# Optimization experiments

Hardware: AMD Instinct MI355X
Metric: run time of the kernel (lower is better)

## Reference

```python
import jax, jax.numpy as jnp
import numpy as np

HEADS = 48
HEAD_DIM = 64
DIM = 3072
RANK = 128
TEXT_LEN = 226
VID_LEN = 1822
B = 1
LORA_W = 1.0
EPS = 1e-5


def setup_inputs() -> dict:
    key = jax.random.key(0)
    ks = jax.random.split(key, 24)
    s = 0.02  # weight init scale
    inp = {
        "hidden_states": jax.random.normal(ks[0], (B, VID_LEN, DIM), jnp.float32),
        "encoder_hidden_states": jax.random.normal(ks[1], (B, TEXT_LEN, DIM), jnp.float32),
        "rope_cos": jax.random.uniform(ks[2], (VID_LEN, HEAD_DIM), jnp.float32),
        "rope_sin": jax.random.uniform(ks[3], (VID_LEN, HEAD_DIM), jnp.float32),
        "Wq": jax.random.normal(ks[4], (DIM, DIM), jnp.float32) * s,
        "bq": jax.random.normal(ks[5], (DIM,), jnp.float32) * s,
        "Wk": jax.random.normal(ks[6], (DIM, DIM), jnp.float32) * s,
        "bk": jax.random.normal(ks[7], (DIM,), jnp.float32) * s,
        "Wv": jax.random.normal(ks[8], (DIM, DIM), jnp.float32) * s,
        "bv": jax.random.normal(ks[9], (DIM,), jnp.float32) * s,
        "Wo": jax.random.normal(ks[10], (DIM, DIM), jnp.float32) * s,
        "bo": jax.random.normal(ks[11], (DIM,), jnp.float32) * s,
        "lq_down": jax.random.normal(ks[12], (RANK, DIM), jnp.float32) / RANK,
        "lq_up": jax.random.normal(ks[13], (DIM, RANK), jnp.float32) * s,
        "lk_down": jax.random.normal(ks[14], (RANK, DIM), jnp.float32) / RANK,
        "lk_up": jax.random.normal(ks[15], (DIM, RANK), jnp.float32) * s,
        "lv_down": jax.random.normal(ks[16], (RANK, DIM), jnp.float32) / RANK,
        "lv_up": jax.random.normal(ks[17], (DIM, RANK), jnp.float32) * s,
        "lp_down": jax.random.normal(ks[18], (RANK, DIM), jnp.float32) / RANK,
        "lp_up": jax.random.normal(ks[19], (DIM, RANK), jnp.float32) * s,
        "gamma_q": jnp.ones((HEAD_DIM,), jnp.float32),
        "beta_q": jnp.zeros((HEAD_DIM,), jnp.float32),
        "gamma_k": jnp.ones((HEAD_DIM,), jnp.float32),
        "beta_k": jnp.zeros((HEAD_DIM,), jnp.float32),
    }
    return inp


def _lora(x, down, up):
    # x: [B,S,DIM]; down: [RANK,DIM]; up: [DIM,RANK]
    return (x @ down.T) @ up.T


def _layernorm(x, gamma, beta):
    mu = jnp.mean(x, axis=-1, keepdims=True)
    var = jnp.mean(jnp.square(x - mu), axis=-1, keepdims=True)
    return (x - mu) * jax.lax.rsqrt(var + EPS) * gamma + beta


def _apply_rope(x, cos, sin):
    # diffusers apply_rotary_emb, use_real=True, unbind_dim=-1
    # x: [B,H,S,D]; cos/sin: [S,D]
    xr = x.reshape(*x.shape[:-1], HEAD_DIM // 2, 2)
    x1, x2 = xr[..., 0], xr[..., 1]
    x_rot = jnp.stack([-x2, x1], axis=-1).reshape(x.shape)
    return x * cos + x_rot * sin


def reference(hidden_states, encoder_hidden_states, rope_cos, rope_sin,
              Wq, bq, Wk, bk, Wv, bv, Wo, bo,
              lq_down, lq_up, lk_down, lk_up, lv_down, lv_up, lp_down, lp_up,
              gamma_q, beta_q, gamma_k, beta_k):
    h = jnp.concatenate([encoder_hidden_states, hidden_states], axis=1)  # [B,S,DIM]
    S = h.shape[1]

    q = h @ Wq.T + bq + _lora(h, lq_down, lq_up) * LORA_W
    k = h @ Wk.T + bk + _lora(h, lk_down, lk_up) * LORA_W
    v = h @ Wv.T + bv + _lora(h, lv_down, lv_up) * LORA_W

    def split_heads(x):  # [B,S,DIM] -> [B,H,S,D]
        return x.reshape(B, S, HEADS, HEAD_DIM).transpose(0, 2, 1, 3)

    q, k, v = split_heads(q), split_heads(k), split_heads(v)
    q = _layernorm(q, gamma_q, beta_q)
    k = _layernorm(k, gamma_k, beta_k)

    # RoPE on video tokens only
    q = q.at[:, :, TEXT_LEN:].set(_apply_rope(q[:, :, TEXT_LEN:], rope_cos, rope_sin))
    k = k.at[:, :, TEXT_LEN:].set(_apply_rope(k[:, :, TEXT_LEN:], rope_cos, rope_sin))

    # scaled dot-product attention (no mask, no dropout)
    scale = 1.0 / np.sqrt(HEAD_DIM).astype(np.float32)
    scores = jnp.einsum("bhqd,bhkd->bhqk", q, k) * scale
    probs = jax.nn.softmax(scores, axis=-1)
    attn_out = jnp.einsum("bhqk,bhkd->bhqd", probs, v)

    out = attn_out.transpose(0, 2, 1, 3).reshape(B, S, DIM)
    out = out @ Wo.T + bo + _lora(out, lp_down, lp_up) * LORA_W

    enc_out = out[:, :TEXT_LEN, :]
    hid_out = out[:, TEXT_LEN:, :]
    return (hid_out, enc_out)
```

## Files before the change

kernel.cpp:

```cpp
#include <hip/hip_runtime.h>
#include <hip/hip_bf16.h>
#include <stdint.h>

#define S_TOT 2048
#define TEXT 226
#define VID 1822
#define DIM 3072
#define NH 48
#define HD 64

typedef __bf16 bf16x8 __attribute__((ext_vector_type(8)));
typedef __bf16 bf16x4 __attribute__((ext_vector_type(4)));
typedef float f32x4 __attribute__((ext_vector_type(4)));

#define AS1 __attribute__((address_space(1)))
#define AS3 __attribute__((address_space(3)))

__device__ __forceinline__ void g2l16(const void* g, void* l) {
    __builtin_amdgcn_global_load_lds((const AS1 uint32_t*)(uintptr_t)g,
                                     (AS3 uint32_t*)(uintptr_t)l, 16, 0, 0);
}

__device__ __forceinline__ f32x4 mfma16(bf16x4 a, bf16x4 b, f32x4 c) {
#if __has_builtin(__builtin_amdgcn_mfma_f32_16x16x16bf16_1k)
    typedef short s4 __attribute__((ext_vector_type(4)));
    union U { bf16x4 b; s4 s; };
    U ua, ub; ua.b = a; ub.b = b;
    return __builtin_amdgcn_mfma_f32_16x16x16bf16_1k(ua.s, ub.s, c, 0, 0, 0);
#else
    f32x4 d = c;
    asm volatile("v_mfma_f32_16x16x16_bf16 %0, %1, %2, %0"
                 : "+v"(d) : "v"(a), "v"(b));
    return d;
#endif
}

#define ARENA_N 47431680ull

struct NormArgs { const void* p[24]; };

__global__ __launch_bounds__(256)
void normalize_inputs(NormArgs a, __bf16* __restrict__ arena)
{
    static constexpr unsigned long long segStart[25] = {
        0ull, 694272ull, 6291456ull, 15728640ull, 25165824ull, 34603008ull,
        44040192ull, 44433408ull, 44826624ull, 45219840ull, 45613056ull,
        46006272ull, 46399488ull, 46792704ull, 47185920ull, 47302528ull,
        47419136ull, 47422208ull, 47425280ull, 47428352ull, 47431424ull,
        47431488ull, 47431552ull, 47431616ull, 47431680ull };
    static constexpr int segIn[24] = {
        1, 0, 4, 6, 8, 10, 12, 13, 14, 15, 16, 17, 18, 19, 2, 3,
        5, 7, 9, 11, 20, 21, 22, 23 };

    const uint32_t w0 = *(const uint32_t*)a.p[20];
    const bool f32in = (w0 == 0x3F800000u);

    const size_t i0 = ((size_t)blockIdx.x * 256 + threadIdx.x) * 8;
    if (i0 >= ARENA_N) return;
    int s = 0;
    while (i0 >= segStart[s + 1]) s++;
    const size_t off = i0 - segStart[s];

    if (f32in) {
        const float* src = (const float*)a.p[segIn[s]] + off;
        const float4 v0 = ((const float4*)src)[0];
        const float4 v1 = ((const float4*)src)[1];
        bf16x8 o;
        o[0] = (__bf16)v0.x; o[1] = (__bf16)v0.y; o[2] = (__bf16)v0.z; o[3] = (__bf16)v0.w;
        o[4] = (__bf16)v1.x; o[5] = (__bf16)v1.y; o[6] = (__bf16)v1.z; o[7] = (__bf16)v1.w;
        *(bf16x8*)(arena + i0) = o;
    } else {
        const __bf16* src = (const __bf16*)a.p[segIn[s]] + off;
        *(uint4*)(arena + i0) = *(const uint4*)src;
    }
}

__device__ __forceinline__ void mm_chunks(
    const __bf16* __restrict__ Ag, int lda, const __bf16* __restrict__ Bg, int ldb,
    int kbeg, int kend, f32x4 (&acc)[4][4], __bf16* As, __bf16* Bs,
    int wave, int srow, int schk, int rdoff, int l15, int wm, int wn)
{
    for (int k0 = kbeg; k0 < kend; k0 += 32) {
        __syncthreads();
#pragma unroll
        for (int i = 0; i < 2; i++) {
            const int blk = i * 4 + wave;
            const int r = blk * 16 + srow;
            g2l16(Ag + (size_t)r * lda + k0 + schk, &As[blk * 512]);
            g2l16(Bg + (size_t)r * ldb + k0 + schk, &Bs[blk * 512]);
        }
        __syncthreads();
        bf16x8 af[4], bfr[4];
#pragma unroll
        for (int i = 0; i < 4; i++)
            af[i] = *(const bf16x8*)&As[(wm + i * 16 + l15) * 32 + rdoff];
#pragma unroll
        for (int j = 0; j < 4; j++)
            bfr[j] = *(const bf16x8*)&Bs[(wn + j * 16 + l15) * 32 + rdoff];
#pragma unroll
        for (int i = 0; i < 4; i++)
#pragma unroll
            for (int j = 0; j < 4; j++)
                acc[i][j] = __builtin_amdgcn_mfma_f32_16x16x32_bf16(af[i], bfr[j], acc[i][j], 0, 0, 0);
    }
}

template<int MODE, bool ATOMIC, bool FUSE2>
__global__ __launch_bounds__(256)
void gemm_bt(const __bf16* __restrict__ A, int lda,
             const __bf16* __restrict__ B0, const __bf16* __restrict__ B1,
             const __bf16* __restrict__ B2, int ldb,
             const __bf16* __restrict__ bias0, const __bf16* __restrict__ bias1,
             const __bf16* __restrict__ bias2,
             const __bf16* __restrict__ A2, int lda2, int a2ColOff,
             const __bf16* __restrict__ U0, const __bf16* __restrict__ U1,
             const __bf16* __restrict__ U2, int ldu,
             float* __restrict__ C, __bf16* __restrict__ Cb, int ldc,
             int K, int K2, int tilesPerGroup, int kChunk,
             void* __restrict__ dout, const void* __restrict__ probe)
{
    __shared__ __bf16 As[128 * 32];
    __shared__ __bf16 Bs[128 * 32];
    const int tid  = threadIdx.x;
    const int wave = tid >> 6;
    const int lane = tid & 63;
    const int l15  = lane & 15, quad = lane >> 4;
    const int bm = blockIdx.x, bn = blockIdx.y;
    const int group = bn / tilesPerGroup;
    const int nt    = bn - group * tilesPerGroup;
    const __bf16* B    = (group == 0) ? B0 : ((group == 1) ? B1 : B2);
    const __bf16* bias = (group == 0) ? bias0 : ((group == 1) ? bias1 : bias2);

    const int k0s = blockIdx.z * kChunk;
    int k0e = k0s + kChunk; if (k0e > K) k0e = K;

    const int srow  = lane >> 2;
    const int schk  = ((((lane & 3) - (lane >> 3)) & 3)) * 8;
    const int rdoff = ((quad + (l15 >> 1)) & 3) * 8;
    const __bf16* Ag = A + (size_t)(bm * 128) * lda;
    const __bf16* Bg = B + (size_t)(nt * 128) * ldb;

    f32x4 acc[4][4] = {};
    const int wm = (wave & 1) * 64;
    const int wn = (wave >> 1) * 64;

    mm_chunks(Ag, lda, Bg, ldb, k0s, k0e, acc, As, Bs, wave, srow, schk, rdoff, l15, wm, wn);

    if (FUSE2) {
        const __bf16* U = (group == 0) ? U0 : ((group == 1) ? U1 : U2);
        const __bf16* A2g = A2 + group * a2ColOff + (size_t)(bm * 128) * lda2;
        const __bf16* Ug  = U + (size_t)(nt * 128) * ldu;
        mm_chunks(A2g, lda2, Ug, ldu, 0, K2, acc, As, Bs, wave, srow, schk, rdoff, l15, wm, wn);
    }

    bool f32out = false;
    if (MODE == 1) f32out = (*(const uint32_t*)probe == 0x3F800000u);

#pragma unroll
    for (int i = 0; i < 4; i++) {
#pragma unroll
        for (int j = 0; j < 4; j++) {
            const int coll = wn + j * 16 + l15;
            const int col  = bn * 128 + coll;
            float bv = 0.f;
            if (bias) bv = (float)bias[nt * 128 + coll];
#pragma unroll
            for (int r = 0; r < 4; r++) {
                const int row = bm * 128 + wm + i * 16 + quad * 4 + r;
                float v = acc[i][j][r] + bv;
                if (MODE == 1) {
                    const size_t mrow = (row < TEXT) ? (size_t)(row + VID) : (size_t)(row - TEXT);
                    if (f32out) ((float*)dout)[mrow * DIM + col] = v;
                    else        ((__bf16*)dout)[mrow * DIM + col] = (__bf16)v;
                } else if (MODE == 3) {
                    Cb[(size_t)row * ldc + col] = (__bf16)v;
                } else if (ATOMIC) {
                    atomicAdd(C + (size_t)row * ldc + col, v);
                } else {
                    C[(size_t)row * ldc + col] = v;
                }
            }
        }
    }
}

__global__ __launch_bounds__(256)
void ln_rope(const __bf16* __restrict__ qkv,
             const __bf16* __restrict__ gq, const __bf16* __restrict__ bq,
             const __bf16* __restrict__ gk, const __bf16* __restrict__ bk,
             const __bf16* __restrict__ cosb, const __bf16* __restrict__ sinb,
             __bf16* __restrict__ qh, __bf16* __restrict__ kh)
{
    const int s = blockIdx.x;
    const int wave = threadIdx.x >> 6, lane = threadIdx.x & 63;
    for (int idx = wave; idx < 2 * NH; idx += 4) {
        const int mat  = idx / NH;
        const int head = idx - mat * NH;
        float x = (float)qkv[(size_t)s * 9216 + mat * DIM + head * HD + lane];
        float mu = x;
        mu += __shfl_xor(mu, 1, 64);  mu += __shfl_xor(mu, 2, 64);
        mu += __shfl_xor(mu, 4, 64);  mu += __shfl_xor(mu, 8, 64);
        mu += __shfl_xor(mu, 16, 64); mu += __shfl_xor(mu, 32, 64);
        mu *= 0.015625f;
        float d = x - mu;
        float vv = d * d;
        vv += __shfl_xor(vv, 1, 64);  vv += __shfl_xor(vv, 2, 64);
        vv += __shfl_xor(vv, 4, 64);  vv += __shfl_xor(vv, 8, 64);
        vv += __shfl_xor(vv, 16, 64); vv += __shfl_xor(vv, 32, 64);
        vv *= 0.015625f;
        const float g = (float)(mat ? gk[lane] : gq[lane]);
        const float b = (float)(mat ? bk[lane] : bq[lane]);
        float y = d * rsqrtf(vv + 1e-5f) * g + b;
        if (s >= TEXT) {
            const int pos = s - TEXT;
            const float c  = (float)cosb[pos * HD + lane];
            const float sn = (float)sinb[pos * HD + lane];
            const float oth = __shfl_xor(y, 1, 64);
            const float rot = (lane & 1) ? oth : -oth;
            y = y * c + rot * sn;
        }
        __bf16* dst = mat ? kh : qh;
        dst[((size_t)head * S_TOT + s) * HD + lane] = (__bf16)y;
    }
}

__global__ __launch_bounds__(256)
void vtrans(const __bf16* __restrict__ qkv, __bf16* __restrict__ vt)
{
    __shared__ float tile[64][65];
    const int h = blockIdx.x, sb = blockIdx.y;
    const int tid = threadIdx.x;
    const int r0 = tid >> 4;
    const int c0 = (tid & 15) * 4;
#pragma unroll
    for (int p = 0; p < 4; p++) {
        const int r = p * 16 + r0;
        const uint2 raw = *(const uint2*)&qkv[((size_t)(sb * 64 + r)) * 9216 + 2 * DIM + h * HD + c0];
        const __bf16* b = (const __bf16*)&raw;
#pragma unroll
        for (int e = 0; e < 4; e++) tile[r][c0 + e] = (float)b[e];
    }
    __syncthreads();
#pragma unroll
    for (int p = 0; p < 4; p++) {
        const int d = p * 16 + r0;
        __bf16 o[4];
#pragma unroll
        for (int e = 0; e < 4; e++) o[e] = (__bf16)tile[c0 + e][d];
        *(uint2*)&vt[((size_t)(h * HD + d)) * S_TOT + sb * 64 + c0] = *(const uint2*)o;
    }
}

#define KS_LD 72
#define VS_LD 136
#define NKB (S_TOT / 128)

__device__ __forceinline__ void fa_load(const __bf16* __restrict__ kh,
                                        const __bf16* __restrict__ vt,
                                        int h, int kb, int tid,
                                        bf16x8 (&kr)[4], bf16x8 (&vr)[4])
{
#pragma unroll
    for (int p = 0; p < 4; p++) {
        const int id = p * 256 + tid;
        const int krow = id >> 3, kc = (id & 7) * 8;
        kr[p] = *(const bf16x8*)(kh + ((size_t)(h * S_TOT + kb * 128 + krow)) * HD + kc);
        const int vrow = id >> 4, vc = (id & 15) * 8;
        vr[p] = *(const bf16x8*)(vt + ((size_t)(h * HD + vrow)) * S_TOT + kb * 128 + vc);
    }
}

__global__ __launch_bounds__(256)
void flash_attn(const __bf16* __restrict__ qh, const __bf16* __restrict__ kh,
                const __bf16* __restrict__ vt, __bf16* __restrict__ outp)
{
    __shared__ __bf16 Ks[128 * KS_LD];
    __shared__ __bf16 Vs[64 * VS_LD];
    const int qb = blockIdx.x, h = blockIdx.y;
    const int tid = threadIdx.x, wave = tid >> 6, lane = tid & 63;
    const int l15 = lane & 15, quad = lane >> 4;

    bf16x8 qf[2][2];
#pragma unroll
    for (int t = 0; t < 2; t++)
#pragma unroll
        for (int ks = 0; ks < 2; ks++) {
            const __bf16* p = qh + ((size_t)(h * S_TOT + qb * 128 + wave * 32 + t * 16 + l15)) * HD
                                 + ks * 32 + quad * 8;
            bf16x8 v = *(const bf16x8*)p;
#pragma unroll
            for (int e = 0; e < 8; e++) v[e] = (__bf16)((float)v[e] * 0.125f);
            qf[t][ks] = v;
        }

    f32x4 of[2][4] = {};
    float m_i[2] = {-1e30f, -1e30f};
    float l_i[2] = {0.f, 0.f};
    const float L2E = 1.44269504f;

    bf16x8 kr[4], vr[4];
    fa_load(kh, vt, h, 0, tid, kr, vr);

    for (int kb = 0; kb < NKB; kb++) {
        __syncthreads();
#pragma unroll
        for (int p = 0; p < 4; p++) {
            const int id = p * 256 + tid;
            const int krow = id >> 3, kc = (id & 7) * 8;
            *(bf16x8*)&Ks[krow * KS_LD + kc] = kr[p];
            const int vrow = id >> 4, vc = (id & 15) * 8;
            *(bf16x8*)&Vs[vrow * VS_LD + vc] = vr[p];
        }
        __syncthreads();
        if (kb + 1 < NKB) fa_load(kh, vt, h, kb + 1, tid, kr, vr);

        bf16x4 pf[2][8];
        float alpha_l[2];
#pragma unroll
        for (int t = 0; t < 2; t++) {
            f32x4 sf[8];
#pragma unroll
            for (int n = 0; n < 8; n++) {
                const bf16x8 k0 = *(const bf16x8*)&Ks[(n * 16 + l15) * KS_LD + quad * 8];
                const bf16x8 k1 = *(const bf16x8*)&Ks[(n * 16 + l15) * KS_LD + 32 + quad * 8];
                f32x4 z = {0.f, 0.f, 0.f, 0.f};
                z = __builtin_amdgcn_mfma_f32_16x16x32_bf16(k0, qf[t][0], z, 0, 0, 0);
                sf[n] = __builtin_amdgcn_mfma_f32_16x16x32_bf16(k1, qf[t][1], z, 0, 0, 0);
            }
            float mx = sf[0][0];
#pragma unroll
            for (int n = 0; n < 8; n++)
#pragma unroll
                for (int r = 0; r < 4; r++) mx = fmaxf(mx, sf[n][r]);
            mx = fmaxf(mx, __shfl_xor(mx, 16, 64));
            mx = fmaxf(mx, __shfl_xor(mx, 32, 64));
            const float mnew = fmaxf(m_i[t], mx);
            alpha_l[t] = __builtin_amdgcn_exp2f((m_i[t] - mnew) * L2E);
            m_i[t] = mnew;
            float rs = 0.f;
#pragma unroll
            for (int n = 0; n < 8; n++)
#pragma unroll
                for (int r = 0; r < 4; r++) {
                    const float pv = __builtin_amdgcn_exp2f((sf[n][r] - mnew) * L2E);
                    sf[n][r] = pv;
                    rs += pv;
                }
            rs += __shfl_xor(rs, 16, 64);
            rs += __shfl_xor(rs, 32, 64);
            l_i[t] = l_i[t] * alpha_l[t] + rs;
#pragma unroll
            for (int kk = 0; kk < 8; kk++) {
                bf16x4 o;
                o[0] = (__bf16)sf[kk][0]; o[1] = (__bf16)sf[kk][1];
                o[2] = (__bf16)sf[kk][2]; o[3] = (__bf16)sf[kk][3];
                pf[t][kk] = o;
            }
        }

#pragma unroll
        for (int t = 0; t < 2; t++)
#pragma unroll
            for (int r = 0; r < 4; r++) {
                const float a_r = __shfl(alpha_l[t], quad * 4 + r, 16);
#pragma unroll
                for (int j = 0; j < 4; j++) of[t][j][r] *= a_r;
            }

#pragma unroll
        for (int kk = 0; kk < 8; kk++) {
#pragma unroll
            for (int j = 0; j < 4; j++) {
                const bf16x4 vf = *(const bf16x4*)&Vs[(j * 16 + l15) * VS_LD + kk * 16 + quad * 4];
                of[0][j] = mfma16(pf[0][kk], vf, of[0][j]);
                of[1][j] = mfma16(pf[1][kk], vf, of[1][j]);
            }
        }
    }

#pragma unroll
    for (int t = 0; t < 2; t++)
#pragma unroll
        for (int r = 0; r < 4; r++) {
            const float lr = __shfl(l_i[t], quad * 4 + r, 16);
            const float inv = 1.f / lr;
            const int row = qb * 128 + wave * 32 + t * 16 + quad * 4 + r;
#pragma unroll
            for (int j = 0; j < 4; j++)
                outp[(size_t)row * DIM + h * HD + j * 16 + l15] = (__bf16)(of[t][j][r] * inv);
        }
}

__global__ __launch_bounds__(256)
void f32_to_bf16(const float* __restrict__ src, __bf16* __restrict__ dst, int n4)
{
    const int i = blockIdx.x * blockDim.x + threadIdx.x;
    if (i < n4) {
        const float4 v = ((const float4*)src)[i];
        __bf16 o[4] = {(__bf16)v.x, (__bf16)v.y, (__bf16)v.z, (__bf16)v.w};
        ((uint2*)dst)[i] = *(const uint2*)o;
    }
}

extern "C" void kernel_launch(void* const* d_in, const int* in_sizes, int n_in,
                              void* d_out, int out_size, void* d_ws, size_t ws_size,
                              hipStream_t stream)
{
    char* ws = (char*)d_ws;
    __bf16* arena = (__bf16*)ws;

    const __bf16* h     = arena + 0;
    const __bf16* Wq    = arena + 6291456;
    const __bf16* Wk    = arena + 15728640;
    const __bf16* Wv    = arena + 25165824;
    const __bf16* Wo    = arena + 34603008;
    const __bf16* lqd   = arena + 44040192;
    const __bf16* lqu   = arena + 44433408;
    const __bf16* lkd   = arena + 44826624;
    const __bf16* lku   = arena + 45219840;
    const __bf16* lvd   = arena + 45613056;
    const __bf16* lvu   = arena + 46006272;
    const __bf16* lpd   = arena + 46399488;
    const __bf16* lpu   = arena + 46792704;
    const __bf16* ropec = arena + 47185920;
    const __bf16* ropes = arena + 47302528;
    const __bf16* bq    = arena + 47419136;
    const __bf16* bk    = arena + 47422208;
    const __bf16* bv    = arena + 47425280;
    const __bf16* bo    = arena + 47428352;
    const __bf16* gq    = arena + 47431424;
    const __bf16* btq   = arena + 47431488;
    const __bf16* gk    = arena + 47431552;
    const __bf16* btk   = arena + 47431616;

    __bf16* qkvb = (__bf16*)(ws + 94863360);
    float*  t32  = (float*)(ws + 132612096);
    __bf16* t16  = (__bf16*)(ws + 136806400);
    __bf16* qh   = (__bf16*)(ws + 138903552);
    __bf16* kh   = (__bf16*)(ws + 151486464);
    __bf16* vt   = (__bf16*)(ws + 164069376);
    __bf16* attn = (__bf16*)(ws + 0);

    NormArgs na;
    for (int i = 0; i < 24; i++) na.p[i] = d_in[i];
    normalize_inputs<<<(unsigned)((ARENA_N / 8 + 255) / 256), 256, 0, stream>>>(na, arena);

    hipMemsetAsync(t32, 0, (size_t)2048 * 512 * 4, stream);

    gemm_bt<0, true, false><<<dim3(16, 3, 8), 256, 0, stream>>>(
        h, DIM, lqd, lkd, lvd, DIM, nullptr, nullptr, nullptr,
        nullptr, 0, 0, nullptr, nullptr, nullptr, 0,
        t32, nullptr, 512, DIM, 0, 1, 384, nullptr, nullptr);
    f32_to_bf16<<<(2048 * 512 / 4 + 255) / 256, 256, 0, stream>>>(t32, t16, 2048 * 512 / 4);

    gemm_bt<3, false, true><<<dim3(16, 72, 1), 256, 0, stream>>>(
        h, DIM, Wq, Wk, Wv, DIM, bq, bk, bv,
        t16, 512, 128, lqu, lku, lvu, 128,
        nullptr, qkvb, 9216, DIM, 128, 24, DIM, nullptr, nullptr);

    ln_rope<<<2048, 256, 0, stream>>>(qkvb, gq, btq, gk, btk, ropec, ropes, qh, kh);
    vtrans<<<dim3(48, 32), 256, 0, stream>>>(qkvb, vt);
    flash_attn<<<dim3(16, 48), 256, 0, stream>>>(qh, kh, vt, attn);

    gemm_bt<0, true, false><<<dim3(16, 1, 16), 256, 0, stream>>>(
        attn, DIM, lpd, lpd, lpd, DIM, nullptr, nullptr, nullptr,
        nullptr, 0, 0, nullptr, nullptr, nullptr, 0,
        t32 + 384, nullptr, 512, DIM, 0, 1, 192, nullptr, nullptr);
    f32_to_bf16<<<(2048 * 512 / 4 + 255) / 256, 256, 0, stream>>>(t32, t16, 2048 * 512 / 4);

    gemm_bt<1, false, true><<<dim3(16, 24, 1), 256, 0, stream>>>(
        attn, DIM, Wo, Wo, Wo, DIM, bo, bo, bo,
        t16 + 384, 512, 0, lpu, lpu, lpu, 128,
        nullptr, nullptr, DIM, DIM, 128, 24, DIM, d_out, d_in[20]);
}
```

Baseline: 719.9 us.

## Replace atomic split-K with plane reduction, halve flash-attn Q tile, prescale Q

```diff
diff --git a/kernel.cpp b/kernel.cpp
--- a/kernel.cpp
+++ b/kernel.cpp
@@ -105,7 +105,9 @@
     }
 }
 
-template<int MODE, bool ATOMIC, bool FUSE2>
+#define PLANE_ELEMS (2048 * 512)
+
+template<int MODE, bool FUSE2>
 __global__ __launch_bounds__(256)
 void gemm_bt(const __bf16* __restrict__ A, int lda,
              const __bf16* __restrict__ B0, const __bf16* __restrict__ B1,
@@ -155,6 +157,7 @@
 
     bool f32out = false;
     if (MODE == 1) f32out = (*(const uint32_t*)probe == 0x3F800000u);
+    float* Cz = (MODE == 0) ? (C + (size_t)blockIdx.z * PLANE_ELEMS) : C;
 
 #pragma unroll
     for (int i = 0; i < 4; i++) {
@@ -174,10 +177,8 @@
                     else        ((__bf16*)dout)[mrow * DIM + col] = (__bf16)v;
                 } else if (MODE == 3) {
                     Cb[(size_t)row * ldc + col] = (__bf16)v;
-                } else if (ATOMIC) {
-                    atomicAdd(C + (size_t)row * ldc + col, v);
                 } else {
-                    C[(size_t)row * ldc + col] = v;
+                    Cz[(size_t)row * ldc + col] = v;
                 }
             }
         }
@@ -219,6 +220,7 @@
             const float rot = (lane & 1) ? oth : -oth;
             y = y * c + rot * sn;
         }
+        if (mat == 0) y *= 0.125f;
         __bf16* dst = mat ? kh : qh;
         dst[((size_t)head * S_TOT + s) * HD + lane] = (__bf16)y;
     }
@@ -280,22 +282,12 @@
     const int tid = threadIdx.x, wave = tid >> 6, lane = tid & 63;
     const int l15 = lane & 15, quad = lane >> 4;
 
-    bf16x8 qf[2][2];
-#pragma unroll
-    for (int t = 0; t < 2; t++)
-#pragma unroll
-        for (int ks = 0; ks < 2; ks++) {
-            const __bf16* p = qh + ((size_t)(h * S_TOT + qb * 128 + wave * 32 + t * 16 + l15)) * HD
-                                 + ks * 32 + quad * 8;
-            bf16x8 v = *(const bf16x8*)p;
-#pragma unroll
-            for (int e = 0; e < 8; e++) v[e] = (__bf16)((float)v[e] * 0.125f);
-            qf[t][ks] = v;
-        }
-
-    f32x4 of[2][4] = {};
-    float m_i[2] = {-1e30f, -1e30f};
-    float l_i[2] = {0.f, 0.f};
+    const __bf16* qp = qh + ((size_t)(h * S_TOT + qb * 64 + wave * 16 + l15)) * HD + quad * 8;
+    const bf16x8 qf0 = *(const bf16x8*)qp;
+    const bf16x8 qf1 = *(const bf16x8*)(qp + 32);
+
+    f32x4 of[4] = {};
+    float m_i = -1e30f, l_i = 0.f;
     const float L2E = 1.44269504f;
 
     bf16x8 kr[4], vr[4];
@@ -314,90 +306,87 @@
         __syncthreads();
         if (kb + 1 < NKB) fa_load(kh, vt, h, kb + 1, tid, kr, vr);
 
-        bf16x4 pf[2][8];
-        float alpha_l[2];
-#pragma unroll
-        for (int t = 0; t < 2; t++) {
-            f32x4 sf[8];
-#pragma unroll
-            for (int n = 0; n < 8; n++) {
-                const bf16x8 k0 = *(const bf16x8*)&Ks[(n * 16 + l15) * KS_LD + quad * 8];
-                const bf16x8 k1 = *(const bf16x8*)&Ks[(n * 16 + l15) * KS_LD + 32 + quad * 8];
-                f32x4 z = {0.f, 0.f, 0.f, 0.f};
-                z = __builtin_amdgcn_mfma_f32_16x16x32_bf16(k0, qf[t][0], z, 0, 0, 0);
-                sf[n] = __builtin_amdgcn_mfma_f32_16x16x32_bf16(k1, qf[t][1], z, 0, 0, 0);
+        f32x4 sf[8];
+#pragma unroll
+        for (int n = 0; n < 8; n++) {
+            const bf16x8 k0 = *(const bf16x8*)&Ks[(n * 16 + l15) * KS_LD + quad * 8];
+            const bf16x8 k1 = *(const bf16x8*)&Ks[(n * 16 + l15) * KS_LD + 32 + quad * 8];
+            f32x4 z = {0.f, 0.f, 0.f, 0.f};
+            z = __builtin_amdgcn_mfma_f32_16x16x32_bf16(k0, qf0, z, 0, 0, 0);
+            sf[n] = __builtin_amdgcn_mfma_f32_16x16x32_bf16(k1, qf1, z, 0, 0, 0);
+        }
+
+        float mx = sf[0][0];
+#pragma unroll
+        for (int n = 0; n < 8; n++)
+#pragma unroll
+            for (int r = 0; r < 4; r++) mx = fmaxf(mx, sf[n][r]);
+        mx = fmaxf(mx, __shfl_xor(mx, 16, 64));
+        mx = fmaxf(mx, __shfl_xor(mx, 32, 64));
+        const float mnew = fmaxf(m_i, mx);
+        const float alpha = __builtin_amdgcn_exp2f((m_i - mnew) * L2E);
+        m_i = mnew;
+        float rs = 0.f;
+#pragma unroll
+        for (int n = 0; n < 8; n++)
+#pragma unroll
+            for (int r = 0; r < 4; r++) {
+                const float pv = __builtin_amdgcn_exp2f((sf[n][r] - mnew) * L2E);
+                sf[n][r] = pv;
+                rs += pv;
             }
-            float mx = sf[0][0];
-#pragma unroll
-            for (int n = 0; n < 8; n++)
-#pragma unroll
-                for (int r = 0; r < 4; r++) mx = fmaxf(mx, sf[n][r]);
-            mx = fmaxf(mx, __shfl_xor(mx, 16, 64));
-            mx = fmaxf(mx, __shfl_xor(mx, 32, 64));
-            const float mnew = fmaxf(m_i[t], mx);
-            alpha_l[t] = __builtin_amdgcn_exp2f((m_i[t] - mnew) * L2E);
-            m_i[t] = mnew;
-            float rs = 0.f;
-#pragma unroll
-            for (int n = 0; n < 8; n++)
-#pragma unroll
-                for (int r = 0; r < 4; r++) {
-                    const float pv = __builtin_amdgcn_exp2f((sf[n][r] - mnew) * L2E);
-                    sf[n][r] = pv;
-                    rs += pv;
-                }
-            rs += __shfl_xor(rs, 16, 64);
-            rs += __shfl_xor(rs, 32, 64);
-            l_i[t] = l_i[t] * alpha_l[t] + rs;
-#pragma unroll
-            for (int kk = 0; kk < 8; kk++) {
-                bf16x4 o;
-                o[0] = (__bf16)sf[kk][0]; o[1] = (__bf16)sf[kk][1];
-                o[2] = (__bf16)sf[kk][2]; o[3] = (__bf16)sf[kk][3];
-                pf[t][kk] = o;
-            }
-        }
-
-#pragma unroll
-        for (int t = 0; t < 2; t++)
-#pragma unroll
-            for (int r = 0; r < 4; r++) {
-                const float a_r = __shfl(alpha_l[t], quad * 4 + r, 16);
-#pragma unroll
-                for (int j = 0; j < 4; j++) of[t][j][r] *= a_r;
-            }
+        rs += __shfl_xor(rs, 16, 64);
+        rs += __shfl_xor(rs, 32, 64);
+        l_i = l_i * alpha + rs;
+
+        bf16x4 pf[8];
+#pragma unroll
+        for (int kk = 0; kk < 8; kk++) {
+            bf16x4 o;
+            o[0] = (__bf16)sf[kk][0]; o[1] = (__bf16)sf[kk][1];
+            o[2] = (__bf16)sf[kk][2]; o[3] = (__bf16)sf[kk][3];
+            pf[kk] = o;
+        }
+
+#pragma unroll
+        for (int r = 0; r < 4; r++) {
+            const float a_r = __shfl(alpha, quad * 4 + r, 16);
+#pragma unroll
+            for (int j = 0; j < 4; j++) of[j][r] *= a_r;
+        }
 
 #pragma unroll
         for (int kk = 0; kk < 8; kk++) {
 #pragma unroll
             for (int j = 0; j < 4; j++) {
                 const bf16x4 vf = *(const bf16x4*)&Vs[(j * 16 + l15) * VS_LD + kk * 16 + quad * 4];
-                of[0][j] = mfma16(pf[0][kk], vf, of[0][j]);
-                of[1][j] = mfma16(pf[1][kk], vf, of[1][j]);
+                of[j] = mfma16(pf[kk], vf, of[j]);
             }
         }
     }
 
 #pragma unroll
-    for (int t = 0; t < 2; t++)
-#pragma unroll
-        for (int r = 0; r < 4; r++) {
-            const float lr = __shfl(l_i[t], quad * 4 + r, 16);
-            const float inv = 1.f / lr;
-            const int row = qb * 128 + wave * 32 + t * 16 + quad * 4 + r;
-#pragma unroll
-            for (int j = 0; j < 4; j++)
-                outp[(size_t)row * DIM + h * HD + j * 16 + l15] = (__bf16)(of[t][j][r] * inv);
-        }
-}
-
-__global__ __launch_bounds__(256)
-void f32_to_bf16(const float* __restrict__ src, __bf16* __restrict__ dst, int n4)
+    for (int r = 0; r < 4; r++) {
+        const float lr = __shfl(l_i, quad * 4 + r, 16);
+        const float inv = 1.f / lr;
+        const int row = qb * 64 + wave * 16 + quad * 4 + r;
+#pragma unroll
+        for (int j = 0; j < 4; j++)
+            outp[(size_t)row * DIM + h * HD + j * 16 + l15] = (__bf16)(of[j][r] * inv);
+    }
+}
+
+__global__ __launch_bounds__(256)
+void reduce4_bf16(const float* __restrict__ src, __bf16* __restrict__ dst, int n4)
 {
     const int i = blockIdx.x * blockDim.x + threadIdx.x;
     if (i < n4) {
-        const float4 v = ((const float4*)src)[i];
-        __bf16 o[4] = {(__bf16)v.x, (__bf16)v.y, (__bf16)v.z, (__bf16)v.w};
+        const float4 a = ((const float4*)src)[i];
+        const float4 b = ((const float4*)(src + PLANE_ELEMS))[i];
+        const float4 c = ((const float4*)(src + 2 * PLANE_ELEMS))[i];
+        const float4 d = ((const float4*)(src + 3 * PLANE_ELEMS))[i];
+        __bf16 o[4] = {(__bf16)(a.x + b.x + c.x + d.x), (__bf16)(a.y + b.y + c.y + d.y),
+                       (__bf16)(a.z + b.z + c.z + d.z), (__bf16)(a.w + b.w + c.w + d.w)};
         ((uint2*)dst)[i] = *(const uint2*)o;
     }
 }
@@ -435,40 +424,38 @@
 
     __bf16* qkvb = (__bf16*)(ws + 94863360);
     float*  t32  = (float*)(ws + 132612096);
-    __bf16* t16  = (__bf16*)(ws + 136806400);
-    __bf16* qh   = (__bf16*)(ws + 138903552);
-    __bf16* kh   = (__bf16*)(ws + 151486464);
-    __bf16* vt   = (__bf16*)(ws + 164069376);
+    __bf16* t16  = (__bf16*)(ws + 149389312);
+    __bf16* qh   = (__bf16*)(ws + 151486464);
+    __bf16* kh   = (__bf16*)(ws + 164069376);
+    __bf16* vt   = (__bf16*)(ws + 176652288);
     __bf16* attn = (__bf16*)(ws + 0);
 
     NormArgs na;
     for (int i = 0; i < 24; i++) na.p[i] = d_in[i];
     normalize_inputs<<<(unsigned)((ARENA_N / 8 + 255) / 256), 256, 0, stream>>>(na, arena);
 
-    hipMemsetAsync(t32, 0, (size_t)2048 * 512 * 4, stream);
-
-    gemm_bt<0, true, false><<<dim3(16, 3, 8), 256, 0, stream>>>(
+    gemm_bt<0, false><<<dim3(16, 3, 4), 256, 0, stream>>>(
         h, DIM, lqd, lkd, lvd, DIM, nullptr, nullptr, nullptr,
         nullptr, 0, 0, nullptr, nullptr, nullptr, 0,
-        t32, nullptr, 512, DIM, 0, 1, 384, nullptr, nullptr);
-    f32_to_bf16<<<(2048 * 512 / 4 + 255) / 256, 256, 0, stream>>>(t32, t16, 2048 * 512 / 4);
-
-    gemm_bt<3, false, true><<<dim3(16, 72, 1), 256, 0, stream>>>(
+        t32, nullptr, 512, DIM, 0, 1, 768, nullptr, nullptr);
+    reduce4_bf16<<<(2048 * 512 / 4 + 255) / 256, 256, 0, stream>>>(t32, t16, 2048 * 512 / 4);
+
+    gemm_bt<3, true><<<dim3(16, 72, 1), 256, 0, stream>>>(
         h, DIM, Wq, Wk, Wv, DIM, bq, bk, bv,
         t16, 512, 128, lqu, lku, lvu, 128,
         nullptr, qkvb, 9216, DIM, 128, 24, DIM, nullptr, nullptr);
 
     ln_rope<<<2048, 256, 0, stream>>>(qkvb, gq, btq, gk, btk, ropec, ropes, qh, kh);
     vtrans<<<dim3(48, 32), 256, 0, stream>>>(qkvb, vt);
-    flash_attn<<<dim3(16, 48), 256, 0, stream>>>(qh, kh, vt, attn);
-
-    gemm_bt<0, true, false><<<dim3(16, 1, 16), 256, 0, stream>>>(
+    flash_attn<<<dim3(32, 48), 256, 0, stream>>>(qh, kh, vt, attn);
+
+    gemm_bt<0, false><<<dim3(16, 1, 4), 256, 0, stream>>>(
         attn, DIM, lpd, lpd, lpd, DIM, nullptr, nullptr, nullptr,
         nullptr, 0, 0, nullptr, nullptr, nullptr, 0,
-        t32 + 384, nullptr, 512, DIM, 0, 1, 192, nullptr, nullptr);
-    f32_to_bf16<<<(2048 * 512 / 4 + 255) / 256, 256, 0, stream>>>(t32, t16, 2048 * 512 / 4);
-
-    gemm_bt<1, false, true><<<dim3(16, 24, 1), 256, 0, stream>>>(
+        t32 + 384, nullptr, 512, DIM, 0, 1, 768, nullptr, nullptr);
+    reduce4_bf16<<<(2048 * 512 / 4 + 255) / 256, 256, 0, stream>>>(t32, t16, 2048 * 512 / 4);
+
+    gemm_bt<1, true><<<dim3(16, 24, 1), 256, 0, stream>>>(
         attn, DIM, Wo, Wo, Wo, DIM, bo, bo, bo,
         t16 + 384, 512, 0, lpu, lpu, lpu, 128,
         nullptr, nullptr, DIM, DIM, 128, 24, DIM, d_out, d_in[20]);
```

Result: no change. 716.7 us (-0.4%).
